# Kernel tuning notes

Measured on AMD Instinct MI355X. Metric: run time of the kernel, lower is better.

The kernel has to match this reference:

```python
import jax, jax.numpy as jnp
import numpy as np

H, D, HID, DIN = 2, 32, 64, 128
NQ, NA, NK = 100000, 200000, 200000
E_KQ, E_QK, E_QA, E_AQ = 800000, 800000, 400000, 400000
EP, EN = 100000, 100000


def setup_inputs() -> dict:
    key = jax.random.key(0)
    ks = jax.random.split(key, 32)
    f = lambda i, shape, s=0.05: jax.random.normal(ks[i], shape, dtype=jnp.float32) * s
    ri = lambda i, n, hi: jax.random.randint(ks[i], (n,), 0, hi)
    return {
        'xq': f(0, (NQ, DIN), 1.0), 'xa': f(1, (NA, DIN), 1.0), 'xk': f(2, (NK, DIN), 1.0),
        'lin_w': f(3, (3, DIN, HID)), 'lin_b': f(4, (3, HID)),
        'k_w': f(5, (3, HID, HID)), 'k_b': f(6, (3, HID)),
        'q_w': f(7, (3, HID, HID)), 'q_b': f(8, (3, HID)),
        'v_w': f(9, (3, HID, HID)), 'v_b': f(10, (3, HID)),
        'a_w': f(11, (3, HID, HID)), 'a_b': f(12, (3, HID)),
        'a_rel': f(13, (4, H, D, D), 0.2), 'm_rel': f(14, (4, H, D, D), 0.2),
        'p_rel': jnp.ones((4, H), dtype=jnp.float32),  # PyG init: ones
        'skip': jnp.ones((3,), dtype=jnp.float32),     # PyG init: ones
        'ei_kq_src': ri(15, E_KQ, NK), 'ei_kq_dst': ri(16, E_KQ, NQ),
        'ei_qk_src': ri(17, E_QK, NQ), 'ei_qk_dst': ri(18, E_QK, NA * 0 + NK),
        'ei_qa_src': ri(19, E_QA, NQ), 'ei_qa_dst': ri(20, E_QA, NA),
        'ei_aq_src': ri(21, E_AQ, NA), 'ei_aq_dst': ri(22, E_AQ, NQ),
        'pos_src': ri(23, EP, NQ), 'pos_dst': ri(24, EP, NA),
        'neg_src': ri(25, EN, NQ), 'neg_dst': ri(26, EN, NA),
    }


def _seg_softmax(alpha, dst, n):
    # softmax over incoming edges per destination node (per head)
    m = jax.ops.segment_max(alpha, dst, num_segments=n)
    m = jnp.where(jnp.isfinite(m), m, 0.0)
    e = jnp.exp(alpha - m[dst])
    s = jax.ops.segment_sum(e, dst, num_segments=n)
    return e / (s[dst] + 1e-16)


def hgt_forward(xq, xa, xk, lin_w, lin_b, k_w, k_b, q_w, q_b, v_w, v_b, a_w, a_b,
                a_rel, m_rel, p_rel, skip, edges):
    # node types: 0=question, 1=answer, 2=knowledge
    xs = [jax.nn.relu(x @ lin_w[i] + lin_b[i]) for i, x in enumerate([xq, xa, xk])]
    ns = [x.shape[0] for x in xs]
    k = [(x @ k_w[i] + k_b[i]).reshape(-1, H, D) for i, x in enumerate(xs)]
    q = [(x @ q_w[i] + q_b[i]).reshape(-1, H, D) for i, x in enumerate(xs)]
    v = [(x @ v_w[i] + v_b[i]).reshape(-1, H, D) for i, x in enumerate(xs)]
    out = [jnp.zeros((n, H, D), dtype=xs[0].dtype) for n in ns]
    scale = 1.0 / jnp.sqrt(jnp.float32(D))
    for st, dt, r, es, ed in edges:
        # per-edge-type head-wise key/value transforms (applied at node level)
        k_rel = jnp.einsum('nhd,hde->nhe', k[st], a_rel[r])
        v_rel = jnp.einsum('nhd,hde->nhe', v[st], m_rel[r])
        alpha = (q[dt][ed] * k_rel[es]).sum(-1) * p_rel[r] * scale  # [E,H]
        a = _seg_softmax(alpha, ed, ns[dt])
        msg = a[:, :, None] * v_rel[es]  # [E,H,D]
        out[dt] = out[dt] + jax.ops.segment_sum(msg, ed, num_segments=ns[dt])
    z = []
    for i in range(3):
        o = jax.nn.gelu(out[i].reshape(-1, H * D), approximate=False) @ a_w[i] + a_b[i]
        beta = jax.nn.sigmoid(skip[i])
        z.append(beta * o + (1.0 - beta) * xs[i])
    return z  # [z_question, z_answer, z_knowledge]; note: HGT.forward never applies self.lin


def reference(xq, xa, xk, lin_w, lin_b, k_w, k_b, q_w, q_b, v_w, v_b, a_w, a_b,
              a_rel, m_rel, p_rel, skip,
              ei_kq_src, ei_kq_dst, ei_qk_src, ei_qk_dst, ei_qa_src, ei_qa_dst,
              ei_aq_src, ei_aq_dst, pos_src, pos_dst, neg_src, neg_dst):
    edges = [
        (2, 0, 0, ei_kq_src, ei_kq_dst),  # knowledge -> question
        (0, 2, 1, ei_qk_src, ei_qk_dst),  # question -> knowledge
        (0, 1, 2, ei_qa_src, ei_qa_dst),  # question -> answer
        (1, 0, 3, ei_aq_src, ei_aq_dst),  # answer -> question
    ]
    zq, za, zk = hgt_forward(xq, xa, xk, lin_w, lin_b, k_w, k_b, q_w, q_b, v_w, v_b,
                             a_w, a_b, a_rel, m_rel, p_rel, skip, edges)
    pos_pred = jax.nn.sigmoid((zq[pos_src] * za[pos_dst]).sum(-1))
    neg_pred = jax.nn.sigmoid((zq[neg_src] * za[neg_dst]).sum(-1))
    return (pos_pred, neg_pred, zq, za, zk)
```

## Files before the change

kernel.cpp:

```cpp
#include <hip/hip_runtime.h>
#include <math.h>

namespace {

constexpr int NQn = 100000, NAn = 200000, NKn = 200000;
constexpr int EPc = 100000, ENc = 100000;
constexpr int ETOT = 2400000, NSEG = 600000;

constexpr long XSB_OFF  = 0;
constexpr long OUTB_OFF = 16000000;
constexpr long QBF_OFF  = 32000000;
constexpr long KV_OFF   = 48000000;
constexpr long ZB_OFF   = 86500000;
constexpr long WTB_OFF  = 96200000;
constexpr long WFB_OFF  = 96250000;
constexpr long INT_OFF  = 96300000;
constexpr long DEG_I  = 0;
constexpr long CUR_I  = 600000;
constexpr long OFFS_I = 1200000;
constexpr long PART_I = 1800064;
constexpr long CSRC_I = 1801088;

constexpr int LINT_U = 0;
constexpr int QT_U   = 24576;
constexpr int AT_U   = 36864;
constexpr int WFT_U  = 49152;

__constant__ long c_rbase[4] = {0, 200000, 300032, 400064};

typedef __attribute__((ext_vector_type(8))) short bf16x8;
typedef __attribute__((ext_vector_type(4))) float f32x4;

__device__ inline f32x4 mfma16(bf16x8 a, bf16x8 b, f32x4 c) {
    return __builtin_amdgcn_mfma_f32_16x16x32_bf16(a, b, c, 0, 0, 0);
}

__device__ inline float gelu_f(float x) {
    return 0.5f * x * (1.0f + erff(x * 0.7071067811865475f));
}
__device__ inline float bf2f(unsigned short u) {
    return __uint_as_float(((unsigned)u) << 16);
}
__device__ inline unsigned short f2bf(float f) {
    unsigned u = __float_as_uint(f);
    return (unsigned short)((u + 0x7fffu + ((u >> 16) & 1u)) >> 16);
}

__device__ inline void type_of_block128(int b, int& t, int& n0) {
    if (b < 782)       { t = 0; n0 = b * 128; }
    else if (b < 2345) { t = 1; n0 = (b - 782) * 128; }
    else               { t = 2; n0 = (b - 2345) * 128; }
}

__device__ inline void stage_out_gelu(unsigned short* lds, const unsigned short* src,
                                      int n0, int n, int tid)
{
    for (int c = tid; c < 128 * 8; c += 256) {
        int row = c >> 3, kc = c & 7;
        int node = n0 + row; if (node > n - 1) node = n - 1;
        uint4 v = *(const uint4*)&src[(long)node * 64 + kc * 8];
        float f0 = gelu_f(bf2f((unsigned short)(v.x & 0xffffu)));
        float f1 = gelu_f(bf2f((unsigned short)(v.x >> 16)));
        float f2 = gelu_f(bf2f((unsigned short)(v.y & 0xffffu)));
        float f3 = gelu_f(bf2f((unsigned short)(v.y >> 16)));
        float f4 = gelu_f(bf2f((unsigned short)(v.z & 0xffffu)));
        float f5 = gelu_f(bf2f((unsigned short)(v.z >> 16)));
        float f6 = gelu_f(bf2f((unsigned short)(v.w & 0xffffu)));
        float f7 = gelu_f(bf2f((unsigned short)(v.w >> 16)));
        uint4 o;
        o.x = (unsigned)f2bf(f0) | ((unsigned)f2bf(f1) << 16);
        o.y = (unsigned)f2bf(f2) | ((unsigned)f2bf(f3) << 16);
        o.z = (unsigned)f2bf(f4) | ((unsigned)f2bf(f5) << 16);
        o.w = (unsigned)f2bf(f6) | ((unsigned)f2bf(f7) << 16);
        int byte = (row * 64 + kc * 8) * 2;
        *(uint4*)((char*)lds + (byte ^ ((row & 7) << 4))) = o;
    }
}

template<int K>
__device__ inline void stage_f32(unsigned short* lds, const float* src,
                                 int n0, int n, int tid)
{
    constexpr int CPR = K / 8;
    for (int c = tid; c < 128 * CPR; c += 256) {
        int row = c / CPR, kc = c % CPR;
        int node = n0 + row; if (node > n - 1) node = n - 1;
        const float* sp = &src[(long)node * K + kc * 8];
        float4 f0 = *(const float4*)sp, f1 = *(const float4*)(sp + 4);
        uint4 v;
        v.x = (unsigned)f2bf(f0.x) | ((unsigned)f2bf(f0.y) << 16);
        v.y = (unsigned)f2bf(f0.z) | ((unsigned)f2bf(f0.w) << 16);
        v.z = (unsigned)f2bf(f1.x) | ((unsigned)f2bf(f1.y) << 16);
        v.w = (unsigned)f2bf(f1.z) | ((unsigned)f2bf(f1.w) << 16);
        int byte = (row * K + kc * 8) * 2;
        *(uint4*)((char*)lds + (byte ^ ((row & 7) << 4))) = v;
    }
}

template<int N, int K>
__device__ inline void stage_w(unsigned short* lds, const unsigned short* wt, int tid)
{
    constexpr int CPR = K / 8;
    for (int c = tid; c < N * CPR; c += 256) {
        int nr = c / CPR, kc = c % CPR;
        uint4 v = *(const uint4*)&wt[nr * K + kc * 8];
        int byte = (nr * K + kc * 8) * 2;
        *(uint4*)((char*)lds + (byte ^ ((nr & 7) << 4))) = v;
    }
}

template<int K, int NF>
__device__ inline void mfma_coreT(const unsigned short* ldsX, const unsigned short* ldsW,
                                  f32x4 (&acc)[2][NF], int lane, int w)
{
    const int lrow = lane & 15, lk = (lane >> 4) * 8;
    #pragma unroll
    for (int ks = 0; ks < K / 32; ++ks) {
        bf16x8 a[2], b[NF];
        #pragma unroll
        for (int mf = 0; mf < 2; ++mf) {
            int row = w * 32 + mf * 16 + lrow;
            int byte = (row * K + ks * 32 + lk) * 2;
            a[mf] = *(const bf16x8*)((const char*)ldsX + (byte ^ ((row & 7) << 4)));
        }
        #pragma unroll
        for (int nf = 0; nf < NF; ++nf) {
            int nr = nf * 16 + lrow;
            int byte = (nr * K + ks * 32 + lk) * 2;
            b[nf] = *(const bf16x8*)((const char*)ldsW + (byte ^ ((nr & 7) << 4)));
        }
        #pragma unroll
        for (int mf = 0; mf < 2; ++mf)
            #pragma unroll
            for (int nf = 0; nf < NF; ++nf)
                acc[mf][nf] = mfma16(b[nf], a[mf], acc[mf][nf]);
    }
}

__global__ void prep_all(const float* __restrict__ lin_w, const float* __restrict__ q_w,
                         const float* __restrict__ a_w,
                         const float* __restrict__ kw, const float* __restrict__ kb,
                         const float* __restrict__ vw, const float* __restrict__ vb,
                         const float* __restrict__ a_rel, const float* __restrict__ m_rel,
                         unsigned short* __restrict__ wtb, float* __restrict__ wfb)
{
    const int tid = threadIdx.x;
    if (blockIdx.x < 4) {
        const int r = blockIdx.x;
        const int st_tab[4] = {2, 0, 0, 1};
        const int st = st_tab[r];
        for (int idx = tid; idx < 8192; idx += 256) {
            int d = idx >> 7, c = idx & 127;
            int i = c >> 1, which = c & 1;
            int h = i >> 5, e = i & 31;
            const float* w   = (which ? vw : kw) + st * 4096;
            const float* rel = (which ? m_rel : a_rel) + r * 2048;
            float s = 0.f;
            #pragma unroll
            for (int c32 = 0; c32 < 32; ++c32)
                s += w[d * 64 + h * 32 + c32] * rel[h * 1024 + c32 * 32 + e];
            wtb[WFT_U + r * 8192 + c * 64 + d] = f2bf(s);
        }
        for (int idx = tid; idx < 128; idx += 256) {
            int i = idx >> 1, which = idx & 1;
            int h = i >> 5, e = i & 31;
            const float* b   = (which ? vb : kb) + st * 64;
            const float* rel = (which ? m_rel : a_rel) + r * 2048;
            float s = 0.f;
            #pragma unroll
            for (int c32 = 0; c32 < 32; ++c32)
                s += b[h * 32 + c32] * rel[h * 1024 + c32 * 32 + e];
            wfb[r * 128 + idx] = s;
        }
    } else {
        int i = (blockIdx.x - 4) * 256 + tid;
        if (i < 24576) {
            int t = i / 8192, rem = i % 8192, nn = rem >> 7, kk = rem & 127;
            wtb[LINT_U + i] = f2bf(lin_w[t * 8192 + kk * 64 + nn]);
        } else if (i < 36864) {
            int j = i - 24576;
            int t = j / 4096, rem = j % 4096, nn = rem >> 6, kk = rem & 63;
            wtb[QT_U + j] = f2bf(q_w[t * 4096 + kk * 64 + nn]);
        } else if (i < 49152) {
            int j = i - 36864;
            int t = j / 4096, rem = j % 4096, nn = rem >> 6, kk = rem & 63;
            wtb[AT_U + j] = f2bf(a_w[t * 4096 + kk * 64 + nn]);
        }
    }
}

__global__ void __launch_bounds__(256)
linqkv_mfma(const float* __restrict__ xq, const float* __restrict__ xa,
            const float* __restrict__ xk, const unsigned short* __restrict__ wtb,
            const float* __restrict__ lin_b, const float* __restrict__ q_b,
            const float* __restrict__ wfb, unsigned short* __restrict__ xsb,
            unsigned short* __restrict__ qbf, unsigned short* __restrict__ kvb)
{
    __shared__ unsigned short ldsX[128 * 128];
    __shared__ unsigned short ldsXS[128 * 64];
    int t, n0; type_of_block128(blockIdx.x, t, n0);
    const int cnt[3] = {NQn, NAn, NKn};
    const long noff[3] = {0, NQn, NQn + NAn};
    const float* X = (t == 0) ? xq : (t == 1) ? xa : xk;
    const int n = cnt[t];
    const int tid = threadIdx.x;
    const int w = tid >> 6, lane = tid & 63;
    const int nodeL = lane & 15, colG = (lane >> 4) * 4;
    const int relA_tab[3] = {1, 3, 0};
    const int rA = relA_tab[t];
    const int nrel = (t == 0) ? 2 : 1;

    stage_w<64, 128>(ldsXS, wtb + LINT_U + t * 8192, tid);
    stage_f32<128>(ldsX, X, n0, n, tid);
    __syncthreads();

    f32x4 acc[2][4] = {};
    mfma_coreT<128, 4>(ldsX, ldsXS, acc, lane, w);
    __syncthreads();

    #pragma unroll
    for (int mf = 0; mf < 2; ++mf) {
        int nl = w * 32 + mf * 16 + nodeL;
        int node = n0 + nl;
        #pragma unroll
        for (int nf = 0; nf < 4; ++nf) {
            int col0 = nf * 16 + colG;
            float4 bv = *(const float4*)&lin_b[t * 64 + col0];
            ushort4 o;
            o.x = f2bf(fmaxf(acc[mf][nf][0] + bv.x, 0.f));
            o.y = f2bf(fmaxf(acc[mf][nf][1] + bv.y, 0.f));
            o.z = f2bf(fmaxf(acc[mf][nf][2] + bv.z, 0.f));
            o.w = f2bf(fmaxf(acc[mf][nf][3] + bv.w, 0.f));
            int byte = (nl * 64 + col0) * 2;
            *(ushort4*)((char*)ldsXS + (byte ^ ((nl & 7) << 4))) = o;
            if (node < n)
                *(ushort4*)&xsb[(noff[t] + node) * 64 + col0] = o;
        }
    }
    stage_w<64, 64>(ldsX, wtb + QT_U + t * 4096, tid);
    __syncthreads();

    {
        f32x4 qa[2][4] = {};
        mfma_coreT<64, 4>(ldsXS, ldsX, qa, lane, w);
        #pragma unroll
        for (int mf = 0; mf < 2; ++mf) {
            int node = n0 + w * 32 + mf * 16 + nodeL;
            if (node < n) {
                #pragma unroll
                for (int nf = 0; nf < 4; ++nf) {
                    int col0 = nf * 16 + colG;
                    float4 bv = *(const float4*)&q_b[t * 64 + col0];
                    ushort4 o;
                    o.x = f2bf(qa[mf][nf][0] + bv.x);
                    o.y = f2bf(qa[mf][nf][1] + bv.y);
                    o.z = f2bf(qa[mf][nf][2] + bv.z);
                    o.w = f2bf(qa[mf][nf][3] + bv.w);
                    *(ushort4*)&qbf[(noff[t] + node) * 64 + col0] = o;
                }
            }
        }
    }

    for (int ri = 0; ri < nrel; ++ri) {
        const int r = (ri == 0) ? rA : 2;
        const long rb = c_rbase[r];
        __syncthreads();
        stage_w<128, 64>(ldsX, wtb + WFT_U + r * 8192, tid);
        __syncthreads();
        f32x4 ka[2][8] = {};
        mfma_coreT<64, 8>(ldsXS, ldsX, ka, lane, w);
        #pragma unroll
        for (int mf = 0; mf < 2; ++mf) {
            int node = n0 + w * 32 + mf * 16 + nodeL;
            if (node < n) {
                #pragma unroll
                for (int nf = 0; nf < 8; ++nf) {
                    int col0 = nf * 16 + colG;
                    float4 bv = *(const float4*)&wfb[r * 128 + col0];
                    ushort4 o;
                    o.x = f2bf(ka[mf][nf][0] + bv.x);
                    o.y = f2bf(ka[mf][nf][1] + bv.y);
                    o.z = f2bf(ka[mf][nf][2] + bv.z);
                    o.w = f2bf(ka[mf][nf][3] + bv.w);
                    *(ushort4*)&kvb[(rb + node) * 128 + col0] = o;
                }
            }
        }
    }
}

__global__ void __launch_bounds__(256)
head_mfma(const unsigned short* __restrict__ outb, const unsigned short* __restrict__ xsb,
          const unsigned short* __restrict__ wtb, const float* __restrict__ a_b,
          const float* __restrict__ skip, float* __restrict__ z,
          unsigned short* __restrict__ zb)
{
    __shared__ unsigned short ldsX[128 * 64];
    __shared__ unsigned short ldsW[64 * 64];
    int t, n0; type_of_block128(blockIdx.x, t, n0);
    const int cnt[3] = {NQn, NAn, NKn};
    const long noff[3] = {0, NQn, NQn + NAn};
    const long zoff[3] = {200000L, 6600000L, 19400000L};
    const int n = cnt[t];
    const int tid = threadIdx.x;

    stage_w<64, 64>(ldsW, wtb + AT_U + t * 4096, tid);
    stage_out_gelu(ldsX, outb + noff[t] * 64, n0, n, tid);
    __syncthreads();

    const int w = tid >> 6, lane = tid & 63;
    f32x4 acc[2][4] = {};
    mfma_coreT<64, 4>(ldsX, ldsW, acc, lane, w);

    const float beta = 1.f / (1.f + expf(-skip[t]));
    const int nodeL = lane & 15, colG = (lane >> 4) * 4;
    #pragma unroll
    for (int mf = 0; mf < 2; ++mf) {
        int node = n0 + w * 32 + mf * 16 + nodeL;
        if (node < n) {
            #pragma unroll
            for (int nf = 0; nf < 4; ++nf) {
                int col0 = nf * 16 + colG;
                float4 bv = *(const float4*)&a_b[t * 64 + col0];
                ushort4 rv = *(const ushort4*)&xsb[(noff[t] + node) * 64 + col0];
                float4 o;
                o.x = beta * (acc[mf][nf][0] + bv.x) + (1.f - beta) * bf2f(rv.x);
                o.y = beta * (acc[mf][nf][1] + bv.y) + (1.f - beta) * bf2f(rv.y);
                o.z = beta * (acc[mf][nf][2] + bv.z) + (1.f - beta) * bf2f(rv.z);
                o.w = beta * (acc[mf][nf][3] + bv.w) + (1.f - beta) * bf2f(rv.w);
                *(float4*)&z[zoff[t] + (long)node * 64 + col0] = o;
                if (t < 2) {
                    ushort4 p;
                    p.x = f2bf(o.x); p.y = f2bf(o.y); p.z = f2bf(o.z); p.w = f2bf(o.w);
                    long zrow = (t == 0) ? (long)node : 100000L + node;
                    *(ushort4*)&zb[zrow * 64 + col0] = p;
                }
            }
        }
    }
}

__global__ void csr_count_all(const int* __restrict__ d0, const int* __restrict__ d1,
                              const int* __restrict__ d2, const int* __restrict__ d3,
                              int* __restrict__ deg)
{
    int gid = blockIdx.x * 256 + threadIdx.x;
    if (gid < 800000)       atomicAdd(&deg[d0[gid]], 1);
    else if (gid < 1600000) atomicAdd(&deg[100000 + d1[gid - 800000]], 1);
    else if (gid < 2000000) atomicAdd(&deg[300000 + d2[gid - 1600000]], 1);
    else if (gid < 2400000) atomicAdd(&deg[500000 + d3[gid - 2000000]], 1);
}

__global__ void csr_fill_all(const int* __restrict__ s0, const int* __restrict__ d0,
                             const int* __restrict__ s1, const int* __restrict__ d1,
                             const int* __restrict__ s2, const int* __restrict__ d2,
                             const int* __restrict__ s3, const int* __restrict__ d3,
                             const int* __restrict__ off, int* __restrict__ cur,
                             int* __restrict__ csrc)
{
    int gid = blockIdx.x * 256 + threadIdx.x;
    int seg, s;
    if (gid < 800000)       { seg = d0[gid];                    s = s0[gid]; }
    else if (gid < 1600000) { seg = 100000 + d1[gid - 800000];  s = s1[gid - 800000]; }
    else if (gid < 2000000) { seg = 300000 + d2[gid - 1600000]; s = s2[gid - 1600000]; }
    else if (gid < 2400000) { seg = 500000 + d3[gid - 2000000]; s = s3[gid - 2000000]; }
    else return;
    int slot = off[seg] + atomicAdd(&cur[seg], 1);
    csrc[slot] = s;
}

__global__ void scan1(const int* __restrict__ in, int* __restrict__ out,
                      int* __restrict__ part, int n)
{
    __shared__ int lds[256];
    const int tid = threadIdx.x;
    const int base = blockIdx.x * 1024 + tid * 4;
    int v[4];
    #pragma unroll
    for (int k = 0; k < 4; ++k) v[k] = (base + k < n) ? in[base + k] : 0;
    int tsum = v[0] + v[1] + v[2] + v[3];
    lds[tid] = tsum;
    __syncthreads();
    for (int off = 1; off < 256; off <<= 1) {
        int t = (tid >= off) ? lds[tid - off] : 0;
        __syncthreads();
        lds[tid] += t;
        __syncthreads();
    }
    int excl = lds[tid] - tsum;
    #pragma unroll
    for (int k = 0; k < 4; ++k) {
        if (base + k < n) out[base + k] = excl;
        excl += v[k];
    }
    if (tid == 255) part[blockIdx.x] = lds[255];
}

__global__ void scan2(int* __restrict__ part, int nb)
{
    __shared__ int lds[256];
    const int tid = threadIdx.x;
    const int base = tid * 4;
    int v[4];
    #pragma unroll
    for (int k = 0; k < 4; ++k) v[k] = (base + k < nb) ? part[base + k] : 0;
    int tsum = v[0] + v[1] + v[2] + v[3];
    lds[tid] = tsum;
    __syncthreads();
    for (int off = 1; off < 256; off <<= 1) {
        int t = (tid >= off) ? lds[tid - off] : 0;
        __syncthreads();
        lds[tid] += t;
        __syncthreads();
    }
    int excl = lds[tid] - tsum;
    #pragma unroll
    for (int k = 0; k < 4; ++k) {
        if (base + k < nb) part[base + k] = excl;
        excl += v[k];
    }
}

__global__ void scan3(int* __restrict__ off, const int* __restrict__ part, int n, int E)
{
    int i = blockIdx.x * 256 + threadIdx.x;
    if (i < n) off[i] += part[i >> 10];
    if (i == 0) off[n] = E;
}

__device__ inline void attn_node(const int* __restrict__ csrc, int begin, int end,
                                 const unsigned short* __restrict__ kvt,
                                 const float qv[4], int j, float res[4])
{
    float ss = 0.f, a0 = 0.f, a1 = 0.f, a2 = 0.f, a3 = 0.f;

    for (int t = begin; t < end; t += 4) {
        bool v1 = (t + 1 < end), v2 = (t + 2 < end), v3 = (t + 3 < end);
        int s0 = csrc[t];
        int s1 = csrc[v1 ? t + 1 : t];
        int s2 = csrc[v2 ? t + 2 : t];
        int s3 = csrc[v3 ? t + 3 : t];
        uint4 k0 = *(const uint4*)(kvt + (long)s0 * 128 + j * 8);
        uint4 k1 = *(const uint4*)(kvt + (long)s1 * 128 + j * 8);
        uint4 k2 = *(const uint4*)(kvt + (long)s2 * 128 + j * 8);
        uint4 k3 = *(const uint4*)(kvt + (long)s3 * 128 + j * 8);

        float p0 = __uint_as_float(k0.x << 16) * qv[0] + __uint_as_float(k0.y << 16) * qv[1]
                 + __uint_as_float(k0.z << 16) * qv[2] + __uint_as_float(k0.w << 16) * qv[3];
        float p1 = __uint_as_float(k1.x << 16) * qv[0] + __uint_as_float(k1.y << 16) * qv[1]
                 + __uint_as_float(k1.z << 16) * qv[2] + __uint_as_float(k1.w << 16) * qv[3];
        float p2 = __uint_as_float(k2.x << 16) * qv[0] + __uint_as_float(k2.y << 16) * qv[1]
                 + __uint_as_float(k2.z << 16) * qv[2] + __uint_as_float(k2.w << 16) * qv[3];
        float p3 = __uint_as_float(k3.x << 16) * qv[0] + __uint_as_float(k3.y << 16) * qv[1]
                 + __uint_as_float(k3.z << 16) * qv[2] + __uint_as_float(k3.w << 16) * qv[3];

        p0 += __shfl_xor(p0, 1);  p1 += __shfl_xor(p1, 1);
        p2 += __shfl_xor(p2, 1);  p3 += __shfl_xor(p3, 1);
        p0 += __shfl_xor(p0, 2);  p1 += __shfl_xor(p1, 2);
        p2 += __shfl_xor(p2, 2);  p3 += __shfl_xor(p3, 2);
        p0 += __shfl_xor(p0, 4);  p1 += __shfl_xor(p1, 4);
        p2 += __shfl_xor(p2, 4);  p3 += __shfl_xor(p3, 4);

        float w0 = exp2f(fminf(p0, 115.f));
        float w1 = v1 ? exp2f(fminf(p1, 115.f)) : 0.f;
        float w2 = v2 ? exp2f(fminf(p2, 115.f)) : 0.f;
        float w3 = v3 ? exp2f(fminf(p3, 115.f)) : 0.f;

        ss += (w0 + w1) + (w2 + w3);
        a0 += w0 * __uint_as_float(k0.x & 0xffff0000u) + w1 * __uint_as_float(k1.x & 0xffff0000u)
            + w2 * __uint_as_float(k2.x & 0xffff0000u) + w3 * __uint_as_float(k3.x & 0xffff0000u);
        a1 += w0 * __uint_as_float(k0.y & 0xffff0000u) + w1 * __uint_as_float(k1.y & 0xffff0000u)
            + w2 * __uint_as_float(k2.y & 0xffff0000u) + w3 * __uint_as_float(k3.y & 0xffff0000u);
        a2 += w0 * __uint_as_float(k0.z & 0xffff0000u) + w1 * __uint_as_float(k1.z & 0xffff0000u)
            + w2 * __uint_as_float(k2.z & 0xffff0000u) + w3 * __uint_as_float(k3.z & 0xffff0000u);
        a3 += w0 * __uint_as_float(k0.w & 0xffff0000u) + w1 * __uint_as_float(k1.w & 0xffff0000u)
            + w2 * __uint_as_float(k2.w & 0xffff0000u) + w3 * __uint_as_float(k3.w & 0xffff0000u);
    }

    float inv = 1.f / (ss + 1e-16f);
    res[0] = a0 * inv; res[1] = a1 * inv; res[2] = a2 * inv; res[3] = a3 * inv;
}

__global__ void __launch_bounds__(256)
attn_all(const int* __restrict__ off, const int* __restrict__ csrc,
         const unsigned short* __restrict__ qbf, const unsigned short* __restrict__ kv,
         const float* __restrict__ prel, float scale, unsigned short* __restrict__ outb)
{
    const int tid = threadIdx.x;
    const int nid = blockIdx.x * 16 + (tid >> 4);
    const int j = tid & 15;
    const int h = j >> 3;
    const float l2e = 1.4426950408889634f;

    long row; int segA, segB = -1; long kbA, kbB = 0; float psA, psB = 0.f;
    if (nid < 100000) {
        row = nid;
        segA = nid;            kbA = c_rbase[0]; psA = prel[0 + h] * scale * l2e;
        segB = 500000 + nid;   kbB = c_rbase[3]; psB = prel[6 + h] * scale * l2e;
    } else if (nid < 300000) {
        int kk = nid - 100000;
        row = 300000 + kk;
        segA = 100000 + kk;    kbA = c_rbase[1]; psA = prel[2 + h] * scale * l2e;
    } else {
        int aa = nid - 300000;
        row = 100000 + aa;
        segA = 300000 + aa;    kbA = c_rbase[2]; psA = prel[4 + h] * scale * l2e;
    }

    ushort4 q4 = *(const ushort4*)&qbf[row * 64 + 4 * j];
    float qraw[4] = {bf2f(q4.x), bf2f(q4.y), bf2f(q4.z), bf2f(q4.w)};

    float res[4];
    {
        float qv[4] = {qraw[0] * psA, qraw[1] * psA, qraw[2] * psA, qraw[3] * psA};
        attn_node(csrc, off[segA], off[segA + 1], kv + kbA * 128, qv, j, res);
    }
    if (segB >= 0) {
        float qv[4] = {qraw[0] * psB, qraw[1] * psB, qraw[2] * psB, qraw[3] * psB};
        float r2[4];
        attn_node(csrc, off[segB], off[segB + 1], kv + kbB * 128, qv, j, r2);
        res[0] += r2[0]; res[1] += r2[1]; res[2] += r2[2]; res[3] += r2[3];
    }

    ushort4 o;
    o.x = f2bf(res[0]); o.y = f2bf(res[1]); o.z = f2bf(res[2]); o.w = f2bf(res[3]);
    *(ushort4*)&outb[row * 64 + 4 * j] = o;
}

__global__ void pred_all(const int* __restrict__ psrc, const int* __restrict__ pdst,
                         const int* __restrict__ nsrc, const int* __restrict__ ndst,
                         const unsigned short* __restrict__ zb, float* __restrict__ out)
{
    int t = blockIdx.x * 256 + threadIdx.x;
    int g = t >> 3, lane = t & 7;
    if (g >= EPc + ENc) return;
    int s, d;
    if (g < EPc) { s = psrc[g]; d = pdst[g]; }
    else         { int gg = g - EPc; s = nsrc[gg]; d = ndst[gg]; }
    uint4 zs = *(const uint4*)&zb[(long)s * 64 + lane * 8];
    uint4 zd = *(const uint4*)&zb[(100000L + d) * 64 + lane * 8];
    float p = 0.f;
    p += bf2f((unsigned short)(zs.x & 0xffffu)) * bf2f((unsigned short)(zd.x & 0xffffu));
    p += bf2f((unsigned short)(zs.x >> 16))     * bf2f((unsigned short)(zd.x >> 16));
    p += bf2f((unsigned short)(zs.y & 0xffffu)) * bf2f((unsigned short)(zd.y & 0xffffu));
    p += bf2f((unsigned short)(zs.y >> 16))     * bf2f((unsigned short)(zd.y >> 16));
    p += bf2f((unsigned short)(zs.z & 0xffffu)) * bf2f((unsigned short)(zd.z & 0xffffu));
    p += bf2f((unsigned short)(zs.z >> 16))     * bf2f((unsigned short)(zd.z >> 16));
    p += bf2f((unsigned short)(zs.w & 0xffffu)) * bf2f((unsigned short)(zd.w & 0xffffu));
    p += bf2f((unsigned short)(zs.w >> 16))     * bf2f((unsigned short)(zd.w >> 16));
    p += __shfl_xor(p, 1);
    p += __shfl_xor(p, 2);
    p += __shfl_xor(p, 4);
    if (lane == 0) out[g] = 1.f / (1.f + expf(-p));
}

}

extern "C" void kernel_launch(void* const* d_in, const int* in_sizes, int n_in,
                              void* d_out, int out_size, void* d_ws, size_t ws_size,
                              hipStream_t stream)
{
    const float* xq    = (const float*)d_in[0];
    const float* xa    = (const float*)d_in[1];
    const float* xk    = (const float*)d_in[2];
    const float* lin_w = (const float*)d_in[3];
    const float* lin_b = (const float*)d_in[4];
    const float* k_w   = (const float*)d_in[5];
    const float* k_b   = (const float*)d_in[6];
    const float* q_w   = (const float*)d_in[7];
    const float* q_b   = (const float*)d_in[8];
    const float* v_w   = (const float*)d_in[9];
    const float* v_b   = (const float*)d_in[10];
    const float* a_w   = (const float*)d_in[11];
    const float* a_b   = (const float*)d_in[12];
    const float* a_rel = (const float*)d_in[13];
    const float* m_rel = (const float*)d_in[14];
    const float* p_rel = (const float*)d_in[15];
    const float* skip  = (const float*)d_in[16];
    const int* esrc[4] = {(const int*)d_in[17], (const int*)d_in[19], (const int*)d_in[21], (const int*)d_in[23]};
    const int* edst[4] = {(const int*)d_in[18], (const int*)d_in[20], (const int*)d_in[22], (const int*)d_in[24]};
    const int* pos_src = (const int*)d_in[25];
    const int* pos_dst = (const int*)d_in[26];
    const int* neg_src = (const int*)d_in[27];
    const int* neg_dst = (const int*)d_in[28];

    float* ws   = (float*)d_ws;
    float* outp = (float*)d_out;
    int*   wi   = (int*)(ws + INT_OFF);
    unsigned short* xsb  = (unsigned short*)(ws + XSB_OFF);
    unsigned short* outb = (unsigned short*)(ws + OUTB_OFF);
    unsigned short* qbf  = (unsigned short*)(ws + QBF_OFF);
    unsigned short* kvb  = (unsigned short*)(ws + KV_OFF);
    unsigned short* zbb  = (unsigned short*)(ws + ZB_OFF);
    unsigned short* wtb  = (unsigned short*)(ws + WTB_OFF);
    float*          wfb  = ws + WFB_OFF;

    hipMemsetAsync(wi + DEG_I, 0, 1200000L * sizeof(int), stream);
    csr_count_all<<<(ETOT + 255) / 256, 256, 0, stream>>>(
        edst[0], edst[1], edst[2], edst[3], wi + DEG_I);
    const int nb = (NSEG + 1023) / 1024;
    scan1<<<nb, 256, 0, stream>>>(wi + DEG_I, wi + OFFS_I, wi + PART_I, NSEG);
    scan2<<<1, 256, 0, stream>>>(wi + PART_I, nb);
    scan3<<<(NSEG + 255) / 256, 256, 0, stream>>>(wi + OFFS_I, wi + PART_I, NSEG, ETOT);
    csr_fill_all<<<(ETOT + 255) / 256, 256, 0, stream>>>(
        esrc[0], edst[0], esrc[1], edst[1], esrc[2], edst[2], esrc[3], edst[3],
        wi + OFFS_I, wi + CUR_I, wi + CSRC_I);

    prep_all<<<196, 256, 0, stream>>>(lin_w, q_w, a_w, k_w, k_b, v_w, v_b,
                                      a_rel, m_rel, wtb, wfb);

    linqkv_mfma<<<3908, 256, 0, stream>>>(xq, xa, xk, wtb, lin_b, q_b, wfb,
                                          xsb, qbf, kvb);

    const float scale = 0.17677669529663687f;
    attn_all<<<31250, 256, 0, stream>>>(wi + OFFS_I, wi + CSRC_I, qbf, kvb,
                                        p_rel, scale, outb);

    head_mfma<<<3908, 256, 0, stream>>>(outb, xsb, wtb, a_b, skip, outp, zbb);

    pred_all<<<(200000 * 8 + 255) / 256, 256, 0, stream>>>(
        pos_src, pos_dst, neg_src, neg_dst, zbb, outp);
}
```

Measured before the change: 636.1 us.

## Split fused lin+QKV kernel into separate lin and QKV kernels; merge prep with CSR count

The fused linear+Q+KV projection kernel is split in two. A lin kernel writes xs in bf16, and a second kernel reloads xs and computes Q and the per-relation K/V projections, with one block per tile per relation. This removes the serial loop over relations inside one block (question blocks did two relations) and lowers LDS use per block, at the cost of an extra global round trip of xs. The weight-prep kernel is also merged with the CSR degree-count kernel to save a launch.

Result: no change. 629.2 us (-1.1%).

```diff
diff --git a/kernel.cpp b/kernel.cpp
--- a/kernel.cpp
+++ b/kernel.cpp
@@ -50,6 +50,20 @@
     if (b < 782)       { t = 0; n0 = b * 128; }
     else if (b < 2345) { t = 1; n0 = (b - 782) * 128; }
     else               { t = 2; n0 = (b - 2345) * 128; }
+}
+
+template<int K>
+__device__ inline void stage_bf16(unsigned short* lds, const unsigned short* src,
+                                  int n0, int n, int tid)
+{
+    constexpr int CPR = K / 8;
+    for (int c = tid; c < 128 * CPR; c += 256) {
+        int row = c / CPR, kc = c % CPR;
+        int node = n0 + row; if (node > n - 1) node = n - 1;
+        uint4 v = *(const uint4*)&src[(long)node * K + kc * 8];
+        int byte = (row * K + kc * 8) * 2;
+        *(uint4*)((char*)lds + (byte ^ ((row & 7) << 4))) = v;
+    }
 }
 
 __device__ inline void stage_out_gelu(unsigned short* lds, const unsigned short* src,
@@ -137,12 +151,15 @@
     }
 }
 
-__global__ void prep_all(const float* __restrict__ lin_w, const float* __restrict__ q_w,
-                         const float* __restrict__ a_w,
-                         const float* __restrict__ kw, const float* __restrict__ kb,
-                         const float* __restrict__ vw, const float* __restrict__ vb,
-                         const float* __restrict__ a_rel, const float* __restrict__ m_rel,
-                         unsigned short* __restrict__ wtb, float* __restrict__ wfb)
+__global__ void prep_count(const float* __restrict__ lin_w, const float* __restrict__ q_w,
+                           const float* __restrict__ a_w,
+                           const float* __restrict__ kw, const float* __restrict__ kb,
+                           const float* __restrict__ vw, const float* __restrict__ vb,
+                           const float* __restrict__ a_rel, const float* __restrict__ m_rel,
+                           unsigned short* __restrict__ wtb, float* __restrict__ wfb,
+                           const int* __restrict__ d0, const int* __restrict__ d1,
+                           const int* __restrict__ d2, const int* __restrict__ d3,
+                           int* __restrict__ deg)
 {
     const int tid = threadIdx.x;
     if (blockIdx.x < 4) {
@@ -172,7 +189,7 @@
                 s += b[h * 32 + c32] * rel[h * 1024 + c32 * 32 + e];
             wfb[r * 128 + idx] = s;
         }
-    } else {
+    } else if (blockIdx.x < 196) {
         int i = (blockIdx.x - 4) * 256 + tid;
         if (i < 24576) {
             int t = i / 8192, rem = i % 8192, nn = rem >> 7, kk = rem & 127;
@@ -186,63 +203,80 @@
             int t = j / 4096, rem = j % 4096, nn = rem >> 6, kk = rem & 63;
             wtb[AT_U + j] = f2bf(a_w[t * 4096 + kk * 64 + nn]);
         }
+    } else {
+        int gid = (blockIdx.x - 196) * 256 + tid;
+        if (gid < 800000)       atomicAdd(&deg[d0[gid]], 1);
+        else if (gid < 1600000) atomicAdd(&deg[100000 + d1[gid - 800000]], 1);
+        else if (gid < 2000000) atomicAdd(&deg[300000 + d2[gid - 1600000]], 1);
+        else if (gid < 2400000) atomicAdd(&deg[500000 + d3[gid - 2000000]], 1);
     }
 }
 
 __global__ void __launch_bounds__(256)
-linqkv_mfma(const float* __restrict__ xq, const float* __restrict__ xa,
-            const float* __restrict__ xk, const unsigned short* __restrict__ wtb,
-            const float* __restrict__ lin_b, const float* __restrict__ q_b,
-            const float* __restrict__ wfb, unsigned short* __restrict__ xsb,
-            unsigned short* __restrict__ qbf, unsigned short* __restrict__ kvb)
+lin_mfma(const float* __restrict__ xq, const float* __restrict__ xa,
+         const float* __restrict__ xk, const unsigned short* __restrict__ wtb,
+         const float* __restrict__ lin_b, unsigned short* __restrict__ xsb)
 {
     __shared__ unsigned short ldsX[128 * 128];
-    __shared__ unsigned short ldsXS[128 * 64];
+    __shared__ unsigned short ldsW[64 * 128];
     int t, n0; type_of_block128(blockIdx.x, t, n0);
     const int cnt[3] = {NQn, NAn, NKn};
     const long noff[3] = {0, NQn, NQn + NAn};
     const float* X = (t == 0) ? xq : (t == 1) ? xa : xk;
     const int n = cnt[t];
     const int tid = threadIdx.x;
+
+    stage_w<64, 128>(ldsW, wtb + LINT_U + t * 8192, tid);
+    stage_f32<128>(ldsX, X, n0, n, tid);
+    __syncthreads();
+
+    const int w = tid >> 6, lane = tid & 63;
+    f32x4 acc[2][4] = {};
+    mfma_coreT<128, 4>(ldsX, ldsW, acc, lane, w);
+
+    const int nodeL = lane & 15, colG = (lane >> 4) * 4;
+    #pragma unroll
+    for (int mf = 0; mf < 2; ++mf) {
+        int node = n0 + w * 32 + mf * 16 + nodeL;
+        if (node < n) {
+            #pragma unroll
+            for (int nf = 0; nf < 4; ++nf) {
+                int col0 = nf * 16 + colG;
+                float4 bv = *(const float4*)&lin_b[t * 64 + col0];
+                ushort4 o;
+                o.x = f2bf(fmaxf(acc[mf][nf][0] + bv.x, 0.f));
+                o.y = f2bf(fmaxf(acc[mf][nf][1] + bv.y, 0.f));
+                o.z = f2bf(fmaxf(acc[mf][nf][2] + bv.z, 0.f));
+                o.w = f2bf(fmaxf(acc[mf][nf][3] + bv.w, 0.f));
+                *(ushort4*)&xsb[(noff[t] + node) * 64 + col0] = o;
+            }
+        }
+    }
+}
+
+__global__ void __launch_bounds__(256)
+qkv_split(const unsigned short* __restrict__ xsb, const unsigned short* __restrict__ wtb,
+          const float* __restrict__ q_b, const float* __restrict__ wfb,
+          unsigned short* __restrict__ qbf, unsigned short* __restrict__ kvb)
+{
+    __shared__ unsigned short ldsX[128 * 64];
+    __shared__ unsigned short ldsW[128 * 64];
+    const int cnt[3] = {NQn, NAn, NKn};
+    const long noff[3] = {0, NQn, NQn + NAn};
+    const int tid = threadIdx.x;
     const int w = tid >> 6, lane = tid & 63;
     const int nodeL = lane & 15, colG = (lane >> 4) * 4;
-    const int relA_tab[3] = {1, 3, 0};
-    const int rA = relA_tab[t];
-    const int nrel = (t == 0) ? 2 : 1;
-
-    stage_w<64, 128>(ldsXS, wtb + LINT_U + t * 8192, tid);
-    stage_f32<128>(ldsX, X, n0, n, tid);
-    __syncthreads();
-
-    f32x4 acc[2][4] = {};
-    mfma_coreT<128, 4>(ldsX, ldsXS, acc, lane, w);
-    __syncthreads();
-
-    #pragma unroll
-    for (int mf = 0; mf < 2; ++mf) {
-        int nl = w * 32 + mf * 16 + nodeL;
-        int node = n0 + nl;
-        #pragma unroll
-        for (int nf = 0; nf < 4; ++nf) {
-            int col0 = nf * 16 + colG;
-            float4 bv = *(const float4*)&lin_b[t * 64 + col0];
-            ushort4 o;
-            o.x = f2bf(fmaxf(acc[mf][nf][0] + bv.x, 0.f));
-            o.y = f2bf(fmaxf(acc[mf][nf][1] + bv.y, 0.f));
-            o.z = f2bf(fmaxf(acc[mf][nf][2] + bv.z, 0.f));
-            o.w = f2bf(fmaxf(acc[mf][nf][3] + bv.w, 0.f));
-            int byte = (nl * 64 + col0) * 2;
-            *(ushort4*)((char*)ldsXS + (byte ^ ((nl & 7) << 4))) = o;
-            if (node < n)
-                *(ushort4*)&xsb[(noff[t] + node) * 64 + col0] = o;
-        }
-    }
-    stage_w<64, 64>(ldsX, wtb + QT_U + t * 4096, tid);
-    __syncthreads();
-
-    {
-        f32x4 qa[2][4] = {};
-        mfma_coreT<64, 4>(ldsXS, ldsX, qa, lane, w);
+    const int b = blockIdx.x;
+
+    if (b < 3908) {
+        int t, n0; type_of_block128(b, t, n0);
+        const int n = cnt[t];
+        stage_bf16<64>(ldsX, xsb + noff[t] * 64, n0, n, tid);
+        stage_w<64, 64>(ldsW, wtb + QT_U + t * 4096, tid);
+        __syncthreads();
+
+        f32x4 acc[2][4] = {};
+        mfma_coreT<64, 4>(ldsX, ldsW, acc, lane, w);
         #pragma unroll
         for (int mf = 0; mf < 2; ++mf) {
             int node = n0 + w * 32 + mf * 16 + nodeL;
@@ -252,24 +286,32 @@
                     int col0 = nf * 16 + colG;
                     float4 bv = *(const float4*)&q_b[t * 64 + col0];
                     ushort4 o;
-                    o.x = f2bf(qa[mf][nf][0] + bv.x);
-                    o.y = f2bf(qa[mf][nf][1] + bv.y);
-                    o.z = f2bf(qa[mf][nf][2] + bv.z);
-                    o.w = f2bf(qa[mf][nf][3] + bv.w);
+                    o.x = f2bf(acc[mf][nf][0] + bv.x);
+                    o.y = f2bf(acc[mf][nf][1] + bv.y);
+                    o.z = f2bf(acc[mf][nf][2] + bv.z);
+                    o.w = f2bf(acc[mf][nf][3] + bv.w);
                     *(ushort4*)&qbf[(noff[t] + node) * 64 + col0] = o;
                 }
             }
         }
-    }
-
-    for (int ri = 0; ri < nrel; ++ri) {
-        const int r = (ri == 0) ? rA : 2;
+    } else {
+        int kb = b - 3908, r, lb;
+        if (kb < 1563)      { r = 0; lb = kb; }
+        else if (kb < 2345) { r = 1; lb = kb - 1563; }
+        else if (kb < 3127) { r = 2; lb = kb - 2345; }
+        else                { r = 3; lb = kb - 3127; }
+        const int stt[4] = {2, 0, 0, 1};
+        const int st = stt[r];
+        const int n0 = lb * 128;
+        const int n = cnt[st];
         const long rb = c_rbase[r];
+
+        stage_bf16<64>(ldsX, xsb + noff[st] * 64, n0, n, tid);
+        stage_w<128, 64>(ldsW, wtb + WFT_U + r * 8192, tid);
         __syncthreads();
-        stage_w<128, 64>(ldsX, wtb + WFT_U + r * 8192, tid);
-        __syncthreads();
-        f32x4 ka[2][8] = {};
-        mfma_coreT<64, 8>(ldsXS, ldsX, ka, lane, w);
+
+        f32x4 acc[2][8] = {};
+        mfma_coreT<64, 8>(ldsX, ldsW, acc, lane, w);
         #pragma unroll
         for (int mf = 0; mf < 2; ++mf) {
             int node = n0 + w * 32 + mf * 16 + nodeL;
@@ -279,10 +321,10 @@
                     int col0 = nf * 16 + colG;
                     float4 bv = *(const float4*)&wfb[r * 128 + col0];
                     ushort4 o;
-                    o.x = f2bf(ka[mf][nf][0] + bv.x);
-                    o.y = f2bf(ka[mf][nf][1] + bv.y);
-                    o.z = f2bf(ka[mf][nf][2] + bv.z);
-                    o.w = f2bf(ka[mf][nf][3] + bv.w);
+                    o.x = f2bf(acc[mf][nf][0] + bv.x);
+                    o.y = f2bf(acc[mf][nf][1] + bv.y);
+                    o.z = f2bf(acc[mf][nf][2] + bv.z);
+                    o.w = f2bf(acc[mf][nf][3] + bv.w);
                     *(ushort4*)&kvb[(rb + node) * 128 + col0] = o;
                 }
             }
@@ -341,17 +383,6 @@
     }
 }
 
-__global__ void csr_count_all(const int* __restrict__ d0, const int* __restrict__ d1,
-                              const int* __restrict__ d2, const int* __restrict__ d3,
-                              int* __restrict__ deg)
-{
-    int gid = blockIdx.x * 256 + threadIdx.x;
-    if (gid < 800000)       atomicAdd(&deg[d0[gid]], 1);
-    else if (gid < 1600000) atomicAdd(&deg[100000 + d1[gid - 800000]], 1);
-    else if (gid < 2000000) atomicAdd(&deg[300000 + d2[gid - 1600000]], 1);
-    else if (gid < 2400000) atomicAdd(&deg[500000 + d3[gid - 2000000]], 1);
-}
-
 __global__ void csr_fill_all(const int* __restrict__ s0, const int* __restrict__ d0,
                              const int* __restrict__ s1, const int* __restrict__ d1,
                              const int* __restrict__ s2, const int* __restrict__ d2,
@@ -597,8 +628,11 @@
     float*          wfb  = ws + WFB_OFF;
 
     hipMemsetAsync(wi + DEG_I, 0, 1200000L * sizeof(int), stream);
-    csr_count_all<<<(ETOT + 255) / 256, 256, 0, stream>>>(
+
+    prep_count<<<196 + 9375, 256, 0, stream>>>(
+        lin_w, q_w, a_w, k_w, k_b, v_w, v_b, a_rel, m_rel, wtb, wfb,
         edst[0], edst[1], edst[2], edst[3], wi + DEG_I);
+
     const int nb = (NSEG + 1023) / 1024;
     scan1<<<nb, 256, 0, stream>>>(wi + DEG_I, wi + OFFS_I, wi + PART_I, NSEG);
     scan2<<<1, 256, 0, stream>>>(wi + PART_I, nb);
@@ -607,11 +641,8 @@
         esrc[0], edst[0], esrc[1], edst[1], esrc[2], edst[2], esrc[3], edst[3],
         wi + OFFS_I, wi + CUR_I, wi + CSRC_I);
 
-    prep_all<<<196, 256, 0, stream>>>(lin_w, q_w, a_w, k_w, k_b, v_w, v_b,
-                                      a_rel, m_rel, wtb, wfb);
-
-    linqkv_mfma<<<3908, 256, 0, stream>>>(xq, xa, xk, wtb, lin_b, q_b, wfb,
-                                          xsb, qbf, kvb);
+    lin_mfma<<<3908, 256, 0, stream>>>(xq, xa, xk, wtb, lin_b, xsb);
+    qkv_split<<<8598, 256, 0, stream>>>(xsb, wtb, q_b, wfb, qbf, kvb);
 
     const float scale = 0.17677669529663687f;
     attn_all<<<31250, 256, 0, stream>>>(wi + OFFS_I, wi + CSRC_I, qbf, kvb,
```
